# Performance work log

Measured on AMD Instinct MI355X. Metric: run time of the kernel, lower is better.

Reference implementation:

```python
import jax, jax.numpy as jnp
import numpy as np

N_NODES = 100000
N_EDGES = 3200000
ALPHA = 0.9
N_LAYERS = 10


def setup_inputs() -> dict:
    key = jax.random.key(0)
    ks = jax.random.split(key, 6)
    x = jax.random.normal(ks[0], (N_NODES, 512), dtype=jnp.float32)
    W_in = jax.random.normal(ks[1], (256, 512), dtype=jnp.float32) * (1.0 / np.sqrt(512))
    b_in = jnp.zeros((256,), dtype=jnp.float32)
    W_out = jax.random.normal(ks[2], (64, 256), dtype=jnp.float32) * (1.0 / np.sqrt(256))
    b_out = jnp.zeros((64,), dtype=jnp.float32)
    edge_index = jax.random.randint(ks[3], (2, N_EDGES), 0, N_NODES, dtype=jnp.int64)
    # ~1/avg_degree scale keeps the iterated propagation numerically stable
    edge_weight = jax.random.uniform(ks[4], (N_EDGES,), dtype=jnp.float32) * (1.0 / 32.0)
    return {"x": x, "W_in": W_in, "b_in": b_in, "W_out": W_out,
            "b_out": b_out, "edge_index": edge_index, "edge_weight": edge_weight}


def _spmm(edge_index, edge_weight, z, n_nodes):
    # out[dst] += w * z[src]  (COO SpMM via gather + segment_sum)
    src, dst = edge_index[0], edge_index[1]
    msg = z[src] * edge_weight[:, None]            # [E, C]
    return jax.ops.segment_sum(msg, dst, num_segments=n_nodes)


def reference(x, W_in, b_in, W_out, b_out, edge_index, edge_weight):
    n_nodes = x.shape[0]
    h = jax.nn.relu(x @ W_in.T + b_in)             # linear_in -> (dropout: eval, identity) -> relu
    z = h @ W_out.T + b_out                        # linear_out: [N, n_classes]
    z0 = z
    for _ in range(N_LAYERS):
        # APPNP propagation: alpha-weighted adj propagation + residual blend with x_0
        z = ALPHA * _spmm(edge_index, edge_weight, z, n_nodes) + (1.0 - ALPHA) * z0
    return z
```

## Files before the change

### kernel.cpp

```cpp
#include <hip/hip_runtime.h>
#include <hip/hip_bf16.h>

typedef __attribute__((ext_vector_type(8))) short bf16x8;
typedef __attribute__((ext_vector_type(4))) float f32x4;

__device__ __forceinline__ short f2b(float f) {
    unsigned u = __builtin_bit_cast(unsigned, f);
    unsigned r = (u + 0x7fffu + ((u >> 16) & 1u)) >> 16;
    return (short)r;
}
__device__ __forceinline__ unsigned f2bu(float f) {
    unsigned u = __builtin_bit_cast(unsigned, f);
    return ((u + 0x7fffu + ((u >> 16) & 1u)) >> 16) & 0xffffu;
}
__device__ __forceinline__ float blo(unsigned u) {
    return __builtin_bit_cast(float, u << 16);
}
__device__ __forceinline__ float bhi(unsigned u) {
    return __builtin_bit_cast(float, u & 0xffff0000u);
}

__global__ __launch_bounds__(256) void wprep(
    const float* __restrict__ W_in, const float* __restrict__ W_out,
    unsigned short* __restrict__ Wi_f, unsigned short* __restrict__ Wo_f)
{
    int o = blockIdx.x * 256 + threadIdx.x;
    if (o < 131072) {
        int j = o & 7, lane = (o >> 3) & 63, t = (o >> 9) & 15, kk = o >> 13;
        int n = t * 16 + (lane & 15);
        int k = kk * 32 + ((lane >> 4) << 3) + j;
        Wi_f[o] = (unsigned short)f2bu(W_in[n * 512 + k]);
    } else if (o < 131072 + 16384) {
        int o2 = o - 131072;
        int j = o2 & 7, lane = (o2 >> 3) & 63, t = (o2 >> 9) & 3, kk2 = o2 >> 11;
        int n = t * 16 + (lane & 15);
        int k = kk2 * 32 + ((lane >> 4) << 3) + j;
        Wo_f[o2] = (unsigned short)f2bu(W_out[n * 256 + k]);
    }
}

__global__ __launch_bounds__(256) void mlp(
    const float* __restrict__ x, const unsigned short* __restrict__ Wi_f,
    const float* __restrict__ b_in, const unsigned short* __restrict__ Wo_f,
    const float* __restrict__ b_out, unsigned short* __restrict__ z0, int M)
{
    __shared__ __align__(16) char smem[33280];
    short* At = (short*)smem;
    short* Bt = (short*)(smem + 5120);
    short* Hs = (short*)smem;

    const int tid  = threadIdx.x;
    const int lane = tid & 63;
    const int w    = tid >> 6;
    const int row0 = blockIdx.x * 64;
    const int c    = lane & 15;
    const int qk   = lane >> 4;

    f32x4 acc[16];
#pragma unroll
    for (int t = 0; t < 16; ++t) { acc[t][0]=0.f; acc[t][1]=0.f; acc[t][2]=0.f; acc[t][3]=0.f; }

    const int f4   = tid & 7;
    const int arow = tid >> 3;
    for (int kk = 0; kk < 16; ++kk) {
        __syncthreads();
#pragma unroll
        for (int p = 0; p < 2; ++p) {
            int row = arow + p * 32;
            int grow = row0 + row;
            float4 v = make_float4(0.f, 0.f, 0.f, 0.f);
            if (grow < M) v = *(const float4*)(x + (size_t)grow * 512 + kk * 32 + f4 * 4);
            uint2 pk;
            pk.x = f2bu(v.x) | (f2bu(v.y) << 16);
            pk.y = f2bu(v.z) | (f2bu(v.w) << 16);
            *(uint2*)(At + row * 40 + f4 * 4) = pk;
        }
#pragma unroll
        for (int i = 0; i < 4; ++i) {
            int t = w * 4 + i;
            const unsigned short* g = Wi_f + (((size_t)kk * 16 + t) * 64 + lane) * 8;
            __builtin_amdgcn_global_load_lds(
                (const __attribute__((address_space(1))) unsigned int*)g,
                (__attribute__((address_space(3))) unsigned int*)(Bt + t * 512),
                16, 0, 0);
        }
        __syncthreads();
        bf16x8 a = *(const bf16x8*)(At + (16 * w + c) * 40 + qk * 8);
#pragma unroll
        for (int t = 0; t < 16; ++t) {
            bf16x8 b = *(const bf16x8*)(Bt + (t * 64 + lane) * 8);
            acc[t] = __builtin_amdgcn_mfma_f32_16x16x32_bf16(a, b, acc[t], 0, 0, 0);
        }
    }
    __syncthreads();
#pragma unroll
    for (int t = 0; t < 16; ++t) {
        int col = 16 * t + c;
        float bv = b_in[col];
        int qb = col >> 3, j = col & 7;
#pragma unroll
        for (int r = 0; r < 4; ++r) {
            int row = 16 * w + qk * 4 + r;
            float h = acc[t][r] + bv;
            h = h > 0.f ? h : 0.f;
            Hs[qb * 520 + row * 8 + j] = f2b(h);
        }
    }
    __syncthreads();
    f32x4 acc2[4];
#pragma unroll
    for (int t = 0; t < 4; ++t) { acc2[t][0]=0.f; acc2[t][1]=0.f; acc2[t][2]=0.f; acc2[t][3]=0.f; }
#pragma unroll
    for (int kk2 = 0; kk2 < 8; ++kk2) {
        bf16x8 a2 = *(const bf16x8*)(Hs + (kk2 * 4 + qk) * 520 + (16 * w + c) * 8);
#pragma unroll
        for (int t = 0; t < 4; ++t) {
            bf16x8 b2 = *(const bf16x8*)(Wo_f + (((size_t)kk2 * 4 + t) * 64 + lane) * 8);
            acc2[t] = __builtin_amdgcn_mfma_f32_16x16x32_bf16(a2, b2, acc2[t], 0, 0, 0);
        }
    }
#pragma unroll
    for (int t = 0; t < 4; ++t) {
        int col = 16 * t + c;
        float bv = b_out[col];
#pragma unroll
        for (int r = 0; r < 4; ++r) {
            int grow = row0 + 16 * w + qk * 4 + r;
            if (grow < M) z0[(size_t)grow * 64 + col] = (unsigned short)f2bu(acc2[t][r] + bv);
        }
    }
}

#define CSR_CH   16384
#define MAXBUK   256

__global__ __launch_bounds__(256) void coarse_hist(
    const int* __restrict__ dst, int* __restrict__ M, int E, int nbuk)
{
    __shared__ int cnt[MAXBUK];
    int tid = threadIdx.x, blk = blockIdx.x;
    for (int i = tid; i < nbuk; i += 256) cnt[i] = 0;
    __syncthreads();
    int e0 = blk * CSR_CH, e1 = e0 + CSR_CH; if (e1 > E) e1 = E;
    for (int e = e0 + tid; e < e1; e += 256) atomicAdd(&cnt[dst[e] >> 9], 1);
    __syncthreads();
    for (int i = tid; i < nbuk; i += 256) M[blk * nbuk + i] = cnt[i];
}

__global__ __launch_bounds__(256) void bucket_scan(
    int* __restrict__ M, int* __restrict__ bucketBase, int nblk, int nbuk)
{
    __shared__ int tot[MAXBUK];
    int tid = threadIdx.x;
    for (int r = tid; r < nbuk; r += 256) {
        int s = 0;
        for (int k = 0; k < nblk; ++k) s += M[k * nbuk + r];
        tot[r] = s;
    }
    __syncthreads();
    if (tid == 0) {
        int s = 0;
        for (int r = 0; r < nbuk; ++r) { int t = tot[r]; tot[r] = s; bucketBase[r] = s; s += t; }
        bucketBase[nbuk] = s;
    }
    __syncthreads();
    for (int r = tid; r < nbuk; r += 256) {
        int s = tot[r];
        for (int k = 0; k < nblk; ++k) { int t = M[k * nbuk + r]; M[k * nbuk + r] = s; s += t; }
    }
}

__global__ __launch_bounds__(256) void coarse_scatter(
    const int* __restrict__ src, const int* __restrict__ dst,
    const float* __restrict__ ew, const int* __restrict__ M,
    int4* __restrict__ tmp, int E, int nbuk)
{
    __shared__ int off[MAXBUK];
    int tid = threadIdx.x, blk = blockIdx.x;
    for (int i = tid; i < nbuk; i += 256) off[i] = M[blk * nbuk + i];
    __syncthreads();
    int e0 = blk * CSR_CH, e1 = e0 + CSR_CH; if (e1 > E) e1 = E;
    for (int e = e0 + tid; e < e1; e += 256) {
        int d = dst[e];
        int pos = atomicAdd(&off[d >> 9], 1);
        tmp[pos] = make_int4(src[e], __builtin_bit_cast(int, ew[e]), d, 0);
    }
}

__global__ __launch_bounds__(256) void fine_sort(
    const int4* __restrict__ tmp, const int* __restrict__ bucketBase,
    int2* __restrict__ csr, int* __restrict__ rowptr, int N, int E)
{
    __shared__ int fc[512];
    __shared__ int fo[512];
    __shared__ int wsum[5];
    int b = blockIdx.x, tid = threadIdx.x;
    int base = bucketBase[b], cnt = bucketBase[b + 1] - base;
    int node0 = b << 9;

    fc[tid] = 0; fc[tid + 256] = 0;
    __syncthreads();
    for (int i = tid; i < cnt; i += 256)
        atomicAdd(&fc[tmp[base + i].z - node0], 1);
    __syncthreads();

    int lane = tid & 63, wid = tid >> 6;
    int runbase = 0;
    for (int h = 0; h < 2; ++h) {
        int v = fc[h * 256 + tid];
        int x = v;
#pragma unroll
        for (int off = 1; off < 64; off <<= 1) { int y = __shfl_up(x, off); if (lane >= off) x += y; }
        if (lane == 63) wsum[wid] = x;
        __syncthreads();
        if (tid == 0) { int s = 0; for (int k = 0; k < 4; ++k) { int t = wsum[k]; wsum[k] = s; s += t; } wsum[4] = s; }
        __syncthreads();
        fo[h * 256 + tid] = runbase + wsum[wid] + x - v;
        runbase += wsum[4];
        __syncthreads();
    }

    for (int i = tid; i < 512; i += 256) {
        int node = node0 + i;
        if (node < N) rowptr[node] = base + fo[i];
    }
    if (b == 0 && tid == 0) rowptr[N] = E;
    __syncthreads();

    for (int i = tid; i < cnt; i += 256) {
        int4 ed = tmp[base + i];
        int pos = atomicAdd(&fo[ed.z - node0], 1);
        csr[base + pos] = make_int2(ed.x, ed.y);
    }
}

__global__ __launch_bounds__(256) void prop_kernel(
    const int* __restrict__ rowptr, const int2* __restrict__ csr,
    const unsigned short* __restrict__ zin, const unsigned short* __restrict__ z0,
    unsigned short* __restrict__ zout_b, float* __restrict__ zout_f,
    int n, int final_layer)
{
    int lane = threadIdx.x & 63;
    int node = blockIdx.x * 4 + (threadIdx.x >> 6);
    if (node >= n) return;
    int beg = rowptr[node], end = rowptr[node + 1];
    const int sub = lane >> 3;
    const int k8  = lane & 7;

    float acc[8];
#pragma unroll
    for (int i = 0; i < 8; ++i) acc[i] = 0.f;

    for (int b = beg; b < end; b += 64) {
        int e = b + lane;
        int2 ed = (e < end) ? csr[e] : make_int2(0, 0);
        int cnt = end - b; if (cnt > 64) cnt = 64;
        int groups = (cnt + 7) >> 3;
        for (int j = 0; j < groups; ++j) {
            int idx = j * 8 + sub;
            int sj = __shfl(ed.x, idx);
            int wb = __shfl(ed.y, idx);
            if (idx < cnt) {
                float wj = __builtin_bit_cast(float, wb);
                uint4 v = *(const uint4*)(zin + (size_t)sj * 64 + k8 * 8);
                acc[0] += wj * blo(v.x); acc[1] += wj * bhi(v.x);
                acc[2] += wj * blo(v.y); acc[3] += wj * bhi(v.y);
                acc[4] += wj * blo(v.z); acc[5] += wj * bhi(v.z);
                acc[6] += wj * blo(v.w); acc[7] += wj * bhi(v.w);
            }
        }
    }
#pragma unroll
    for (int off = 8; off < 64; off <<= 1) {
#pragma unroll
        for (int i = 0; i < 8; ++i) acc[i] += __shfl_xor(acc[i], off);
    }
    if (sub == 0) {
        uint4 zv = *(const uint4*)(z0 + (size_t)node * 64 + k8 * 8);
        float o0 = 0.9f * acc[0] + 0.1f * blo(zv.x);
        float o1 = 0.9f * acc[1] + 0.1f * bhi(zv.x);
        float o2 = 0.9f * acc[2] + 0.1f * blo(zv.y);
        float o3 = 0.9f * acc[3] + 0.1f * bhi(zv.y);
        float o4 = 0.9f * acc[4] + 0.1f * blo(zv.z);
        float o5 = 0.9f * acc[5] + 0.1f * bhi(zv.z);
        float o6 = 0.9f * acc[6] + 0.1f * blo(zv.w);
        float o7 = 0.9f * acc[7] + 0.1f * bhi(zv.w);
        if (final_layer) {
            float* dp = zout_f + (size_t)node * 64 + k8 * 8;
            *(float4*)dp       = make_float4(o0, o1, o2, o3);
            *(float4*)(dp + 4) = make_float4(o4, o5, o6, o7);
        } else {
            uint4 pv;
            pv.x = f2bu(o0) | (f2bu(o1) << 16);
            pv.y = f2bu(o2) | (f2bu(o3) << 16);
            pv.z = f2bu(o4) | (f2bu(o5) << 16);
            pv.w = f2bu(o6) | (f2bu(o7) << 16);
            *(uint4*)(zout_b + (size_t)node * 64 + k8 * 8) = pv;
        }
    }
}

static inline size_t align_up(size_t v, size_t a) { return (v + a - 1) & ~(a - 1); }

extern "C" void kernel_launch(void* const* d_in, const int* in_sizes, int n_in,
                              void* d_out, int out_size, void* d_ws, size_t ws_size,
                              hipStream_t stream)
{
    const float* x     = (const float*)d_in[0];
    const float* W_in  = (const float*)d_in[1];
    const float* b_in  = (const float*)d_in[2];
    const float* W_out = (const float*)d_in[3];
    const float* b_out = (const float*)d_in[4];
    const int*   ei    = (const int*)d_in[5];
    const float* ew    = (const float*)d_in[6];

    const int N = in_sizes[0] / 512;
    const int E = in_sizes[6];
    const int* e_src = ei;
    const int* e_dst = ei + E;

    const int nbuk = (N + 511) >> 9;
    const int nblk = (E + CSR_CH - 1) / CSR_CH;

    char* p = (char*)d_ws;
    size_t zbytes = align_up((size_t)N * 64 * sizeof(unsigned short), 256);
    unsigned short* z0b = (unsigned short*)p; p += zbytes;
    unsigned short* Wi_f = (unsigned short*)p; p += align_up(131072 * 2, 256);
    unsigned short* Wo_f = (unsigned short*)p; p += align_up(16384 * 2, 256);
    int2* csr   = (int2*)p; p += align_up((size_t)E * 8, 256);
    int* rowptr = (int*)p;  p += align_up((size_t)(N + 1) * 4, 256);
    int* M      = (int*)p;  p += align_up((size_t)nblk * nbuk * 4, 256);
    int* bucketBase = (int*)p; p += align_up((size_t)(nbuk + 1) * 4, 256);
    int4* tmp   = (int4*)p; p += align_up((size_t)E * 16, 256);
    unsigned short* zA = (unsigned short*)tmp;
    unsigned short* zB = zA + (size_t)N * 64;

    wprep<<<(131072 + 16384 + 255) / 256, 256, 0, stream>>>(W_in, W_out, Wi_f, Wo_f);
    mlp<<<(N + 63) / 64, 256, 0, stream>>>(x, Wi_f, b_in, Wo_f, b_out, z0b, N);

    coarse_hist<<<nblk, 256, 0, stream>>>(e_dst, M, E, nbuk);
    bucket_scan<<<1, 256, 0, stream>>>(M, bucketBase, nblk, nbuk);
    coarse_scatter<<<nblk, 256, 0, stream>>>(e_src, e_dst, ew, M, tmp, E, nbuk);
    fine_sort<<<nbuk, 256, 0, stream>>>(tmp, bucketBase, csr, rowptr, N, E);

    float* out_f = (float*)d_out;
    int pgrid = (N + 3) / 4;
    for (int i = 0; i < 10; ++i) {
        const unsigned short* zin = (i == 0) ? z0b : ((i & 1) ? zA : zB);
        unsigned short* zoutb = (i & 1) ? zB : zA;
        prop_kernel<<<pgrid, 256, 0, stream>>>(rowptr, csr, zin, z0b,
                                               zoutb, out_f, N, (i == 9) ? 1 : 0);
    }
}
```

Baseline: 1.181 ms.

## Double-buffer MLP weight tiles and batch gathers in SpMM propagation

The MLP kernel now loads x directly into registers in MFMA A-fragment layout, dropping the LDS staging, and double-buffers the W_in tiles in LDS so the next k-slice loads while the current one computes. That leaves one barrier per iteration instead of two. The SpMM kernel reads CSR edges with nontemporal loads and issues four independent row gathers per group before accumulating, which adds memory-level parallelism. Out-of-range edges are padded with a zero weight and a row-0 gather, so short rows do some wasted loads.

```diff
diff --git a/kernel.cpp b/kernel.cpp
--- a/kernel.cpp
+++ b/kernel.cpp
@@ -45,9 +45,9 @@
     const float* __restrict__ b_out, unsigned short* __restrict__ z0, int M)
 {
     __shared__ __align__(16) char smem[33280];
-    short* At = (short*)smem;
-    short* Bt = (short*)(smem + 5120);
-    short* Hs = (short*)smem;
+    short* Bt0 = (short*)smem;
+    short* Bt1 = (short*)(smem + 16384);
+    short* Hs  = (short*)smem;
 
     const int tid  = threadIdx.x;
     const int lane = tid & 63;
@@ -56,43 +56,57 @@
     const int c    = lane & 15;
     const int qk   = lane >> 4;
 
+    const int growA = row0 + 16 * w + c;
+    const float* xrow = x + (size_t)(growA < M ? growA : (M - 1)) * 512 + qk * 8;
+
     f32x4 acc[16];
 #pragma unroll
     for (int t = 0; t < 16; ++t) { acc[t][0]=0.f; acc[t][1]=0.f; acc[t][2]=0.f; acc[t][3]=0.f; }
 
-    const int f4   = tid & 7;
-    const int arow = tid >> 3;
+    float4 av0 = *(const float4*)(xrow);
+    float4 av1 = *(const float4*)(xrow + 4);
+#pragma unroll
+    for (int i = 0; i < 4; ++i) {
+        int t = w * 4 + i;
+        const unsigned short* g = Wi_f + ((size_t)t * 64 + lane) * 8;
+        __builtin_amdgcn_global_load_lds(
+            (const __attribute__((address_space(1))) unsigned int*)g,
+            (__attribute__((address_space(3))) unsigned int*)(Bt0 + t * 512),
+            16, 0, 0);
+    }
+    __syncthreads();
+
     for (int kk = 0; kk < 16; ++kk) {
+        short* Bc = (kk & 1) ? Bt1 : Bt0;
+        short* Bn = (kk & 1) ? Bt0 : Bt1;
+        float4 a0 = av0, a1 = av1;
+        if (kk < 15) {
+            const float* xn = xrow + (kk + 1) * 32;
+            av0 = *(const float4*)(xn);
+            av1 = *(const float4*)(xn + 4);
+#pragma unroll
+            for (int i = 0; i < 4; ++i) {
+                int t = w * 4 + i;
+                const unsigned short* g = Wi_f + (((size_t)(kk + 1) * 16 + t) * 64 + lane) * 8;
+                __builtin_amdgcn_global_load_lds(
+                    (const __attribute__((address_space(1))) unsigned int*)g,
+                    (__attribute__((address_space(3))) unsigned int*)(Bn + t * 512),
+                    16, 0, 0);
+            }
+        }
+        bf16x8 a;
+        a[0] = (short)f2bu(a0.x); a[1] = (short)f2bu(a0.y);
+        a[2] = (short)f2bu(a0.z); a[3] = (short)f2bu(a0.w);
+        a[4] = (short)f2bu(a1.x); a[5] = (short)f2bu(a1.y);
+        a[6] = (short)f2bu(a1.z); a[7] = (short)f2bu(a1.w);
+#pragma unroll
+        for (int t = 0; t < 16; ++t) {
+            bf16x8 b = *(const bf16x8*)(Bc + (t * 64 + lane) * 8);
+            acc[t] = __builtin_amdgcn_mfma_f32_16x16x32_bf16(a, b, acc[t], 0, 0, 0);
+        }
         __syncthreads();
-#pragma unroll
-        for (int p = 0; p < 2; ++p) {
-            int row = arow + p * 32;
-            int grow = row0 + row;
-            float4 v = make_float4(0.f, 0.f, 0.f, 0.f);
-            if (grow < M) v = *(const float4*)(x + (size_t)grow * 512 + kk * 32 + f4 * 4);
-            uint2 pk;
-            pk.x = f2bu(v.x) | (f2bu(v.y) << 16);
-            pk.y = f2bu(v.z) | (f2bu(v.w) << 16);
-            *(uint2*)(At + row * 40 + f4 * 4) = pk;
-        }
-#pragma unroll
-        for (int i = 0; i < 4; ++i) {
-            int t = w * 4 + i;
-            const unsigned short* g = Wi_f + (((size_t)kk * 16 + t) * 64 + lane) * 8;
-            __builtin_amdgcn_global_load_lds(
-                (const __attribute__((address_space(1))) unsigned int*)g,
-                (__attribute__((address_space(3))) unsigned int*)(Bt + t * 512),
-                16, 0, 0);
-        }
-        __syncthreads();
-        bf16x8 a = *(const bf16x8*)(At + (16 * w + c) * 40 + qk * 8);
-#pragma unroll
-        for (int t = 0; t < 16; ++t) {
-            bf16x8 b = *(const bf16x8*)(Bt + (t * 64 + lane) * 8);
-            acc[t] = __builtin_amdgcn_mfma_f32_16x16x32_bf16(a, b, acc[t], 0, 0, 0);
-        }
-    }
-    __syncthreads();
+    }
+
 #pragma unroll
     for (int t = 0; t < 16; ++t) {
         int col = 16 * t + c;
@@ -253,20 +267,33 @@
 
     for (int b = beg; b < end; b += 64) {
         int e = b + lane;
-        int2 ed = (e < end) ? csr[e] : make_int2(0, 0);
+        long long edp = (e < end)
+            ? __builtin_nontemporal_load((const long long*)csr + e)
+            : 0ll;
+        int edx = (int)(edp & 0xffffffffll);
+        int edy = (int)(edp >> 32);
         int cnt = end - b; if (cnt > 64) cnt = 64;
-        int groups = (cnt + 7) >> 3;
-        for (int j = 0; j < groups; ++j) {
-            int idx = j * 8 + sub;
-            int sj = __shfl(ed.x, idx);
-            int wb = __shfl(ed.y, idx);
-            if (idx < cnt) {
-                float wj = __builtin_bit_cast(float, wb);
-                uint4 v = *(const uint4*)(zin + (size_t)sj * 64 + k8 * 8);
-                acc[0] += wj * blo(v.x); acc[1] += wj * bhi(v.x);
-                acc[2] += wj * blo(v.y); acc[3] += wj * bhi(v.y);
-                acc[4] += wj * blo(v.z); acc[5] += wj * bhi(v.z);
-                acc[6] += wj * blo(v.w); acc[7] += wj * bhi(v.w);
+        int nq = (cnt + 31) >> 5;
+        for (int g = 0; g < nq; ++g) {
+            int sj[4]; float wj[4];
+#pragma unroll
+            for (int q = 0; q < 4; ++q) {
+                int idx = g * 32 + q * 8 + sub;
+                sj[q] = __shfl(edx, idx);
+                int wb = __shfl(edy, idx);
+                wj[q] = (idx < cnt) ? __builtin_bit_cast(float, wb) : 0.f;
+            }
+            uint4 v[4];
+#pragma unroll
+            for (int q = 0; q < 4; ++q)
+                v[q] = *(const uint4*)(zin + (size_t)sj[q] * 64 + k8 * 8);
+#pragma unroll
+            for (int q = 0; q < 4; ++q) {
+                float w_ = wj[q];
+                acc[0] += w_ * blo(v[q].x); acc[1] += w_ * bhi(v[q].x);
+                acc[2] += w_ * blo(v[q].y); acc[3] += w_ * bhi(v[q].y);
+                acc[4] += w_ * blo(v[q].z); acc[5] += w_ * bhi(v[q].z);
+                acc[6] += w_ * blo(v[q].w); acc[7] += w_ * bhi(v[q].w);
             }
         }
     }
```

Result: slower. 1.213 ms (+2.7%).
